# Optimization experiments

Measured on AMD Instinct MI355X. Metric: run time of the kernel, lower is better.

The kernel has to match this reference:

```python
import jax, jax.numpy as jnp
import numpy as np

L = 4096   # num_tokens (one prefill sequence)
D = 2048   # hidden_size
HK = 16    # num_k_heads
HV = 32    # num_v_heads
DK = 128   # head_k_dim
DV = 128   # head_v_dim
RATIO = HV // HK
EPS = 1e-6


def setup_inputs() -> dict:
    key = jax.random.key(0)
    ks = jax.random.split(key, 11)
    s = 0.02
    return {
        "hidden_states": jax.random.normal(ks[0], (L, D), jnp.float32),
        "Wq": jax.random.normal(ks[1], (D, HK * DK), jnp.float32) * s,
        "Wk": jax.random.normal(ks[2], (D, HK * DK), jnp.float32) * s,
        "Wv": jax.random.normal(ks[3], (D, HV * DV), jnp.float32) * s,
        "Wz": jax.random.normal(ks[4], (D, HV * DV), jnp.float32) * s,
        "Wb": jax.random.normal(ks[5], (D, HV), jnp.float32) * s,
        "Wa": jax.random.normal(ks[6], (D, HV), jnp.float32) * s,
        "A_log": jnp.log(jax.random.uniform(ks[7], (HV,), jnp.float32, 1.0, 16.0)),
        "dt_bias": jax.random.normal(ks[8], (HV,), jnp.float32) * 0.5,
        "norm_weight": jnp.ones((DV,), jnp.float32),
        "W_out": jax.random.normal(ks[9], (HV * DV, D), jnp.float32) * s,
    }


def _l2norm(x):
    return x * jax.lax.rsqrt(jnp.sum(x * x, axis=-1, keepdims=True) + EPS)


def reference(hidden_states, Wq, Wk, Wv, Wz, Wb, Wa, A_log, dt_bias, norm_weight, W_out):
    h = hidden_states
    # --- input projections (qkvz + ba split) ---
    q = _l2norm((h @ Wq).reshape(L, HK, DK))            # [L, HK, DK]
    k = _l2norm((h @ Wk).reshape(L, HK, DK))
    v = (h @ Wv).reshape(L, HV, DV)                     # [L, HV, DV]
    z = (h @ Wz).reshape(L, HV, DV)                     # gate for RMSNorm
    beta = jax.nn.sigmoid(h @ Wb)                       # [L, HV]
    g = -jnp.exp(A_log) * jax.nn.softplus(h @ Wa + dt_bias)  # [L, HV]
    decay = jnp.exp(g)                                  # per-token per-head decay
    # repeat shared q/k heads to value heads (GQA ratio)
    q = jnp.repeat(q, RATIO, axis=1) * (DK ** -0.5)     # [L, HV, DK]
    k = jnp.repeat(k, RATIO, axis=1)

    # --- gated delta rule recurrence over tokens ---
    def step(S, xs):
        q_t, k_t, v_t, b_t, d_t = xs                    # [HV,DK],[HV,DK],[HV,DV],[HV],[HV]
        S = S * d_t[:, None, None]                      # decay state [HV, DK, DV]
        pred = jnp.einsum('hk,hkv->hv', k_t, S)         # memory readout
        delta = (v_t - pred) * b_t[:, None]             # delta-rule correction
        S = S + k_t[:, :, None] * delta[:, None, :]
        o = jnp.einsum('hk,hkv->hv', q_t, S)
        return S, o

    S0 = jnp.zeros((HV, DK, DV), jnp.float32)
    _, core = jax.lax.scan(step, S0, (q, k, v, beta, decay))  # core: [L, HV, DV]

    # --- gated RMSNorm: x * silu(z), rms-normalize over head dim ---
    x = core * jax.nn.silu(z)
    x = x * jax.lax.rsqrt(jnp.mean(x * x, axis=-1, keepdims=True) + EPS) * norm_weight

    # --- output projection ---
    return x.reshape(L, HV * DV) @ W_out                # [L, D]
```

## Files before the change

kernel.cpp:

```cpp
#include <hip/hip_runtime.h>

#define LTOK 4096
#define DHID 2048
#define HKN  16
#define HVN  32
#define DKK  128
#define NTOT 12288

typedef unsigned short u16;
typedef __attribute__((ext_vector_type(8))) short short8;
typedef __attribute__((ext_vector_type(8))) unsigned short u16x8;
typedef __attribute__((ext_vector_type(4))) unsigned short u16x4;
typedef __attribute__((ext_vector_type(4))) float f32x4;

__device__ __forceinline__ float b2f(u16 u) {
  unsigned int x = ((unsigned int)u) << 16;
  return __builtin_bit_cast(float, x);
}
__device__ __forceinline__ u16 f2bf(float f) {
  unsigned int u = __builtin_bit_cast(unsigned int, f);
  u += 0x7FFFu + ((u >> 16) & 1u);
  return (u16)(u >> 16);
}

template<int C> __device__ __forceinline__ float dppmv(float x) {
  int i = __builtin_amdgcn_update_dpp(0, __builtin_bit_cast(int, x), C, 0xF, 0xF, true);
  return __builtin_bit_cast(float, i);
}
__device__ __forceinline__ float red16(float x) {
  x += dppmv<0xB1>(x);
  x += dppmv<0x4E>(x);
  x += dppmv<0x124>(x);
  x += dppmv<0x128>(x);
  return x;
}

__device__ __forceinline__ void gld16(const void* g, void* l) {
  __builtin_amdgcn_global_load_lds((const __attribute__((address_space(1))) void*)g,
                                   (__attribute__((address_space(3))) void*)l, 16, 0, 0);
}

template<int OFF> __device__ __forceinline__ short8 dsr(unsigned a) {
  short8 r;
  asm volatile("ds_read_b128 %0, %1 offset:%2" : "=v"(r) : "v"(a), "n"(OFF));
  return r;
}
__device__ __forceinline__ short8 gldx4(const u16* p) {
  short8 r;
  asm volatile("global_load_dwordx4 %0, %1, off" : "=v"(r) : "v"(p));
  return r;
}
#define KEEPV(x) asm volatile("" :: "v"(x))

__device__ __forceinline__ int sw16(int r, int c, int rowc) { return (r * rowc + c) ^ ((r & 7) << 3); }

__device__ __forceinline__ void cstore(u16* C, size_t i, float v) { C[i] = f2bf(v); }
__device__ __forceinline__ void cstore(float* C, size_t i, float v) { C[i] = v; }

__global__ __launch_bounds__(256)
void k_cvt(const float* __restrict__ s, u16* __restrict__ d, int n) {
  const int i = (blockIdx.x * 256 + threadIdx.x) * 4;
  const float4 v = *(const float4*)(s + i);
  ushort4 o;
  o.x = f2bf(v.x); o.y = f2bf(v.y); o.z = f2bf(v.z); o.w = f2bf(v.w);
  *(ushort4*)(d + i) = o;
}

__global__ __launch_bounds__(256)
void k_trf(const float* __restrict__ W, u16* __restrict__ Bf, int Ncols, int nkt, int j16base) {
  const int wv = threadIdx.x >> 6, lane = threadIdx.x & 63;
  const int frag = blockIdx.x * 4 + wv;
  const int j16 = frag / nkt, kt = frag % nkt;
  const int r0 = kt * 32 + (lane >> 4) * 8;
  const int c = j16 * 16 + (lane & 15);
  u16x8 o;
#pragma unroll
  for (int e = 0; e < 8; ++e) o[e] = f2bf(W[(size_t)(r0 + e) * Ncols + c]);
  *(u16x8*)(Bf + ((size_t)(j16base + j16) * nkt + kt) * 512 + lane * 8) = o;
}

#define MFMA16(a, b, c) __builtin_amdgcn_mfma_f32_16x16x32_bf16(a, b, c, 0, 0, 0)

template<typename OutT, int NWM, int NWN>
__global__ __launch_bounds__(NWM * 256, 2)
void k_g256(const u16* __restrict__ A, const u16* __restrict__ Bf, OutT* __restrict__ C,
            int M, int N, int K, int NT) {
  constexpr int BN = NWN * 64;
  constexpr int BUFE = NWM * 4096;
  __shared__ u16 Lds[4 * BUFE];
  const int tid = threadIdx.x;
  const int lane = tid & 63, w = tid >> 6;
  const int fr = lane & 15, fq = lane >> 4;
  const int wm = (w >> 2) * 128, wn = (w & 3) * (NWN * 16);
  const int nkt = K >> 5;
  const size_t sK = (size_t)K;

  const int MT = gridDim.x / NT;
  const int nts = (NT < 16) ? NT : 16;
  const int per_super = MT * nts;
  const int super = blockIdx.x / per_super;
  const int within = blockIdx.x % per_super;
  const int mtg = MT >> 3;
  const int q = within >> 3;
  const int mt = (within & 7) * mtg + (q % mtg);
  const int nt = super * nts + q / mtg;

  const int kslot = ((tid & 3) ^ ((tid >> 3) & 3)) * 8;
  const u16* aS = A + (size_t)(mt * (NWM * 128) + (tid >> 2)) * sK + kslot;

  const int jw = nt * (BN / 16) + (w & 3) * NWN;
  const u16* bp[NWN];
#pragma unroll
  for (int j = 0; j < NWN; ++j) bp[j] = Bf + ((size_t)(jw + j) * nkt) * 512 + lane * 8;

  f32x4 acc[8][NWN] = {};

  auto STAGE = [&](int kt_) {
    const int sk = (kt_ < nkt) ? kt_ : nkt - 1;
    u16* base = &Lds[(kt_ & 3) * BUFE];
    gld16(aS + (size_t)sk * 32, base + tid * 8);
    gld16(aS + (size_t)(NWM * 64) * sK + (size_t)sk * 32, base + NWM * 2048 + tid * 8);
  };

#define LOADB(bset, kt_) {                                                    \
    const int sk2 = ((kt_) < nkt) ? (kt_) : (nkt - 1);                        \
    _Pragma("unroll")                                                         \
    for (int j = 0; j < NWN; ++j) bset[j] = gldx4(bp[j] + (size_t)sk2 * 512); }

  const int akey = (fr >> 1) & 3;
  const unsigned ldsBase = (unsigned)(size_t)(__attribute__((address_space(3))) void*)&Lds[0];
  const unsigned aA0 = ldsBase + 2u * (unsigned)((wm + fr) * 32 + ((fq ^ akey) << 3));

  short8 afA[8], afB[8], bs0[NWN], bs1[NWN];

#define RD(afX, kt_) {                                                        \
    const unsigned aAr = aA0 + (unsigned)(((kt_) & 3) * (BUFE * 2));          \
    afX[0] = dsr<0>(aAr);    afX[1] = dsr<1024>(aAr);                         \
    afX[2] = dsr<2048>(aAr); afX[3] = dsr<3072>(aAr);                         \
    afX[4] = dsr<4096>(aAr); afX[5] = dsr<5120>(aAr);                         \
    afX[6] = dsr<6144>(aAr); afX[7] = dsr<7168>(aAr); }

  STAGE(0); STAGE(1); STAGE(2);
  LOADB(bs0, 0)
  LOADB(bs1, 1)
  asm volatile("s_waitcnt vmcnt(0)" ::: "memory");
  __builtin_amdgcn_s_barrier();
  RD(afA, 0)
  asm volatile("s_waitcnt lgkmcnt(0)" ::: "memory");
  __builtin_amdgcn_sched_barrier(0);

#define ITER(kt_, afC, bC, afN) {                                             \
    STAGE((kt_) + 3);                                                         \
    asm volatile("s_waitcnt vmcnt(%0)" :: "n"(NWN + 4) : "memory");           \
    __builtin_amdgcn_s_barrier();                                             \
    __builtin_amdgcn_sched_barrier(0);                                        \
    RD(afN, (kt_) + 1)                                                        \
    __builtin_amdgcn_sched_barrier(0);                                        \
    __builtin_amdgcn_s_setprio(1);                                            \
    _Pragma("unroll")                                                         \
    for (int i = 0; i < 8; ++i)                                               \
      _Pragma("unroll")                                                       \
      for (int j = 0; j < NWN; ++j)                                           \
        acc[i][j] = MFMA16(afC[i], bC[j], acc[i][j]);                         \
    __builtin_amdgcn_s_setprio(0);                                            \
    LOADB(bC, (kt_) + 2)                                                      \
    asm volatile("s_waitcnt lgkmcnt(0)" ::: "memory");                        \
    __builtin_amdgcn_sched_barrier(0); }

  for (int kt = 0; kt < nkt; kt += 2) {
    ITER(kt, afA, bs0, afB)
    ITER(kt + 1, afB, bs1, afA)
  }
#undef ITER
#undef RD
#undef LOADB

  asm volatile("s_waitcnt vmcnt(0) lgkmcnt(0)" ::: "memory");
  __builtin_amdgcn_sched_barrier(0);
  KEEPV(bs0[0]); KEEPV(bs0[1]);
  if constexpr (NWN == 4) { KEEPV(bs0[2]); KEEPV(bs0[3]); }
  KEEPV(bs1[0]); KEEPV(bs1[1]);
  if constexpr (NWN == 4) { KEEPV(bs1[2]); KEEPV(bs1[3]); }
  KEEPV(afA[0]); KEEPV(afA[1]); KEEPV(afA[2]); KEEPV(afA[3]);
  KEEPV(afA[4]); KEEPV(afA[5]); KEEPV(afA[6]); KEEPV(afA[7]);
  KEEPV(afB[0]); KEEPV(afB[1]); KEEPV(afB[2]); KEEPV(afB[3]);
  KEEPV(afB[4]); KEEPV(afB[5]); KEEPV(afB[6]); KEEPV(afB[7]);

  const int r0 = mt * (NWM * 128) + wm + fq * 4;
  const int c0 = nt * BN + wn + fr;
#pragma unroll
  for (int i = 0; i < 8; ++i)
#pragma unroll
    for (int j = 0; j < NWN; ++j)
#pragma unroll
      for (int e = 0; e < 4; ++e)
        cstore(C, (size_t)(r0 + i * 16 + e) * N + c0 + j * 16, acc[i][j][e]);
}

__global__ __launch_bounds__(256)
void k_ba(const float* __restrict__ h, const float* __restrict__ Wb, const float* __restrict__ Wa,
          const float* __restrict__ A_log, const float* __restrict__ dtb,
          float* __restrict__ beta, float* __restrict__ g_out) {
  const int w = threadIdx.x >> 6, lane = threadIdx.x & 63;
  const int t = blockIdx.x * 4 + w;
  const int j = lane & 31;
  const bool isB = lane < 32;
  const float* __restrict__ hr = h + (size_t)t * DHID;
  const float* Wc = isB ? Wb : Wa;
  float acc = 0.f;
  for (int kk = 0; kk < DHID; ++kk) acc = fmaf(hr[kk], Wc[(size_t)kk * HVN + j], acc);
  if (isB) {
    beta[(size_t)t * HVN + j] = 1.f / (1.f + expf(-acc));
  } else {
    float xx = acc + dtb[j];
    float sp = (xx > 20.f) ? xx : log1pf(expf(xx));
    g_out[(size_t)t * HVN + j] = -expf(A_log[j]) * sp;
  }
}

__global__ __launch_bounds__(256)
void k_l2n(u16* __restrict__ qkvz) {
  const int w = threadIdx.x >> 6, lane = threadIdx.x & 63;
  const int r = blockIdx.x * 4 + w;
  const int isK = r >> 16;
  const int rr = r & 65535;
  const int t = rr >> 4, hd = rr & 15;
  u16* p = qkvz + (size_t)t * NTOT + isK * 2048 + hd * DKK + lane * 2;
  float a = b2f(p[0]), b = b2f(p[1]);
  float ss = a * a + b * b;
  ss = red16(ss);
  ss += __shfl_xor(ss, 16);
  ss += __shfl_xor(ss, 32);
  const float sc = rsqrtf(ss + 1e-6f) * (isK ? 1.f : 0.08838834764831845f);
  p[0] = f2bf(a * sc); p[1] = f2bf(b * sc);
}

__global__ __launch_bounds__(256)
void k_r1(const u16* __restrict__ qkvz, const float* __restrict__ beta_g,
          const float* __restrict__ g_g, u16* __restrict__ UM_g, float* __restrict__ cumL_g) {
  const int pair = blockIdx.x;
  const int hv = pair >> 6, n = pair & 63;
  const int hk = hv >> 1;
  const int t0 = n * 64;
  const int tid = threadIdx.x, lane = tid & 63, wv = tid >> 6;
  const int fr = lane & 15, fq = lane >> 4;

  __shared__ __align__(16) u16 Xb[256 * 64];
  __shared__ __align__(16) u16 Dbuf0[64 * 64 * 2];
  __shared__ __align__(16) u16 Dbuf1[64 * 64 * 2];
  __shared__ float Lc[64];
  __shared__ float Bc[64];
  u16* Kl = Dbuf0;

  const int j = tid & 63, h = tid >> 6;
  const u16* kg = qkvz + (size_t)(t0 + j) * NTOT + 2048 + hk * DKK + h * 32;
  const u16* vg = qkvz + (size_t)(t0 + j) * NTOT + 4096 + hv * DKK + h * 32;
  u16x8 kv[4], vv[4];
#pragma unroll
  for (int i = 0; i < 4; ++i) { kv[i] = *(const u16x8*)(kg + i * 8); vv[i] = *(const u16x8*)(vg + i * 8); }
  if (tid < 64) {
    Lc[tid] = g_g[(size_t)(t0 + tid) * HVN + hv];
    Bc[tid] = beta_g[(size_t)(t0 + tid) * HVN + hv];
  }
#pragma unroll
  for (int i = 0; i < 4; ++i) *(u16x8*)&Kl[sw16(j, h * 32 + i * 8, 128)] = kv[i];
  __syncthreads();
  if (tid == 0) { float a = 0.f; for (int t = 0; t < 64; ++t) { a += Lc[t]; Lc[t] = a; } }
  __syncthreads();
  if (tid < 64) cumL_g[(size_t)pair * 64 + tid] = Lc[tid];

  {
    const float bj = Bc[j];
    const float mj = bj * __expf(Lc[j]);
#pragma unroll
    for (int i = 0; i < 4; ++i)
#pragma unroll
      for (int e = 0; e < 8; ++e) {
        int c = h * 32 + i * 8 + e;
        Xb[sw16(c, j, 64)] = f2bf(bj * b2f(vv[i][e]));
        Xb[sw16(128 + c, j, 64)] = f2bf(mj * b2f(kv[i][e]));
      }
  }
  f32x4 kk[4] = {};
#pragma unroll
  for (int ks = 0; ks < 4; ++ks) {
    short8 afr = *(const short8*)&Kl[sw16(wv * 16 + fr, ks * 32 + fq * 8, 128)];
#pragma unroll
    for (int ct = 0; ct < 4; ++ct) {
      short8 bfr = *(const short8*)&Kl[sw16(ct * 16 + fr, ks * 32 + fq * 8, 128)];
      kk[ct] = MFMA16(afr, bfr, kk[ct]);
    }
  }
  __syncthreads();

  f32x4 acc[16];
#pragma unroll
  for (int ct = 0; ct < 16; ++ct) {
    u16x4 xi = *(const u16x4*)&Xb[sw16(ct * 16 + fr, wv * 16 + fq * 4, 64)];
    acc[ct][0] = b2f(xi[0]); acc[ct][1] = b2f(xi[1]); acc[ct][2] = b2f(xi[2]); acc[ct][3] = b2f(xi[3]);
  }
#pragma unroll
  for (int ct = 0; ct < 4; ++ct) {
    const int s = ct * 16 + fr;
    u16x4 pk;
#pragma unroll
    for (int e = 0; e < 4; ++e) {
      const int t = wv * 16 + fq * 4 + e;
      float v = (s < t) ? -Bc[t] * __expf(Lc[t] - Lc[s]) * kk[ct][e] : 0.f;
      pk[e] = f2bf(v);
      Dbuf0[sw16(t, s, 64)] = pk[e];
    }
    *(u16x4*)&Dbuf0[4096 + sw16(s, wv * 16 + fq * 4, 64)] = pk;
  }
  __syncthreads();

  u16* DA = Dbuf0;
  u16* DB = Dbuf1;
  for (int stg = 0; stg < 6; ++stg) {
    u16* Dr = DA;
    u16* Dc = DA + 4096;
    short8 da0 = *(const short8*)&Dr[sw16(wv * 16 + fr, 0 + fq * 8, 64)];
    short8 da1 = *(const short8*)&Dr[sw16(wv * 16 + fr, 32 + fq * 8, 64)];
#pragma unroll
    for (int ct = 0; ct < 16; ++ct) {
      short8 b0 = *(const short8*)&Xb[sw16(ct * 16 + fr, 0 + fq * 8, 64)];
      short8 b1 = *(const short8*)&Xb[sw16(ct * 16 + fr, 32 + fq * 8, 64)];
      acc[ct] = MFMA16(da0, b0, acc[ct]);
      acc[ct] = MFMA16(da1, b1, acc[ct]);
    }
    f32x4 sq[4] = {};
    if (stg < 5) {
#pragma unroll
      for (int ct = 0; ct < 4; ++ct) {
        short8 sb0 = *(const short8*)&Dc[sw16(ct * 16 + fr, 0 + fq * 8, 64)];
        short8 sb1 = *(const short8*)&Dc[sw16(ct * 16 + fr, 32 + fq * 8, 64)];
        sq[ct] = MFMA16(da0, sb0, sq[ct]);
        sq[ct] = MFMA16(da1, sb1, sq[ct]);
      }
    }
    __syncthreads();
#pragma unroll
    for (int ct = 0; ct < 16; ++ct) {
      u16x4 pk;
      pk[0] = f2bf(acc[ct][0]); pk[1] = f2bf(acc[ct][1]); pk[2] = f2bf(acc[ct][2]); pk[3] = f2bf(acc[ct][3]);
      *(u16x4*)&Xb[sw16(ct * 16 + fr, wv * 16 + fq * 4, 64)] = pk;
    }
    if (stg < 5) {
#pragma unroll
      for (int ct = 0; ct < 4; ++ct) {
        u16x4 pk;
        pk[0] = f2bf(sq[ct][0]); pk[1] = f2bf(sq[ct][1]); pk[2] = f2bf(sq[ct][2]); pk[3] = f2bf(sq[ct][3]);
        *(u16x4*)&(DB + 4096)[sw16(ct * 16 + fr, wv * 16 + fq * 4, 64)] = pk;
#pragma unroll
        for (int e = 0; e < 4; ++e) DB[sw16(wv * 16 + fq * 4 + e, ct * 16 + fr, 64)] = pk[e];
      }
    }
    __syncthreads();
    u16* tmp = DA; DA = DB; DB = tmp;
  }

#pragma unroll
  for (int ct = 0; ct < 16; ++ct) {
    const int c = ct * 16 + fr;
#pragma unroll
    for (int e = 0; e < 4; ++e) {
      const int t = wv * 16 + fq * 4 + e;
      float v = acc[ct][e];
      if (ct >= 8) v = -v;
      UM_g[((size_t)pair * 64 + t) * 256 + c] = f2bf(v);
    }
  }
}

__global__ __launch_bounds__(512)
void k_r2(u16* __restrict__ qkvz, const u16* __restrict__ UM_g,
          const float* __restrict__ cumL_g, u16* __restrict__ o1_g) {
  const int hv = blockIdx.x >> 2, cs = blockIdx.x & 3;
  const int hk = hv >> 1;
  const int tid = threadIdx.x, lane = tid & 63, w = tid >> 6;
  const int fr = lane & 15, fq = lane >> 4;
  const int j = tid & 63, h = tid >> 6;
  const int tw = w & 3, dwv = w >> 2;

  __shared__ __align__(16) u16 Ml2[2][8192];
  __shared__ __align__(16) u16 Ql2[2][8192];
  __shared__ __align__(16) u16 Kt2[2][8192];
  __shared__ __align__(16) u16 dT[2048];
  __shared__ __align__(16) u16 SbT[4096];
  __shared__ __align__(16) u16 o1b[2048];
  __shared__ float Lc2[2][64];

  f32x4 sacc[2];
#pragma unroll
  for (int d = 0; d < 2; ++d) sacc[d] = (f32x4){0.f, 0.f, 0.f, 0.f};
  for (int i = tid; i < 4096; i += 512) SbT[i] = 0;

  u16x8 pQ0, pQ1, pK0, pK1, pM0, pM1;
  u16 pUn0, pUn1, pUn2, pUn3, pUc0, pUc1, pUc2, pUc3;
  float pL, pL63;

#define PREF(nn) {                                                            \
    const int nc = ((nn) < 64) ? (nn) : 63;                                   \
    const int pr = hv * 64 + nc; const int tt0 = nc * 64;                     \
    const u16* qg = qkvz + (size_t)(tt0 + j) * NTOT + hk * DKK + h * 16;      \
    pQ0 = *(const u16x8*)qg;          pQ1 = *(const u16x8*)(qg + 8);          \
    pK0 = *(const u16x8*)(qg + 2048); pK1 = *(const u16x8*)(qg + 2056);       \
    const u16* mg = UM_g + ((size_t)pr * 64 + j) * 256;                       \
    pM0 = *(const u16x8*)(mg + 128 + h * 16);                                 \
    pM1 = *(const u16x8*)(mg + 136 + h * 16);                                 \
    const u16* ug = UM_g + ((size_t)pr * 64 + tw * 16 + fq * 4) * 256         \
                    + cs * 32 + dwv * 16 + fr;                                \
    pUn0 = ug[0]; pUn1 = ug[256]; pUn2 = ug[512]; pUn3 = ug[768];             \
    pL = cumL_g[(size_t)pr * 64 + j]; pL63 = cumL_g[(size_t)pr * 64 + 63]; }

#define STW(b) {                                                              \
    *(u16x8*)&Ql2[b][sw16(j, h * 16, 128)] = pQ0;                             \
    *(u16x8*)&Ql2[b][sw16(j, h * 16 + 8, 128)] = pQ1;                         \
    *(u16x8*)&Ml2[b][sw16(j, h * 16, 128)] = pM0;                             \
    *(u16x8*)&Ml2[b][sw16(j, h * 16 + 8, 128)] = pM1;                         \
    const float scK = __expf(pL63 - pL);                                      \
    _Pragma("unroll")                                                         \
    for (int e = 0; e < 8; ++e) {                                             \
      Kt2[b][sw16(h * 16 + e, j, 64)] = f2bf(scK * b2f(pK0[e]));              \
      Kt2[b][sw16(h * 16 + 8 + e, j, 64)] = f2bf(scK * b2f(pK1[e]));          \
    }                                                                         \
    if (h == 0) Lc2[b][j] = pL; }

  PREF(0)
  STW(0)
  __syncthreads();

  for (int n = 0; n < 64; ++n) {
    const int cur = n & 1;
    const int pair = hv * 64 + n, t0 = n * 64;
    pUc0 = pUn0; pUc1 = pUn1; pUc2 = pUn2; pUc3 = pUn3;
    const float curL63 = pL63;
    PREF(n + 1)

    short8 amf[4], aqf[4];
#pragma unroll
    for (int ks = 0; ks < 4; ++ks) {
      amf[ks] = *(const short8*)&Ml2[cur][sw16(tw * 16 + fr, ks * 32 + fq * 8, 128)];
      aqf[ks] = *(const short8*)&Ql2[cur][sw16(tw * 16 + fr, ks * 32 + fq * 8, 128)];
    }
    float el[4];
#pragma unroll
    for (int e = 0; e < 4; ++e) el[e] = __expf(Lc2[cur][tw * 16 + fq * 4 + e]);
    {
      f32x4 dc;
      dc[0] = b2f(pUc0); dc[1] = b2f(pUc1); dc[2] = b2f(pUc2); dc[3] = b2f(pUc3);
      f32x4 oc = {};
#pragma unroll
      for (int ks = 0; ks < 4; ++ks) {
        short8 bs = *(const short8*)&SbT[sw16(dwv * 16 + fr, ks * 32 + fq * 8, 128)];
        dc = MFMA16(amf[ks], bs, dc);
        oc = MFMA16(aqf[ks], bs, oc);
      }
      u16x4 pkd;
      pkd[0] = f2bf(dc[0]); pkd[1] = f2bf(dc[1]); pkd[2] = f2bf(dc[2]); pkd[3] = f2bf(dc[3]);
      *(u16x4*)&dT[sw16(dwv * 16 + fr, tw * 16 + fq * 4, 64)] = pkd;
      u16x4 pko;
#pragma unroll
      for (int e = 0; e < 4; ++e) pko[e] = f2bf(oc[e] * el[e]);
      *(u16x4*)&o1b[sw16(dwv * 16 + fr, tw * 16 + fq * 4, 64)] = pko;
    }
    __syncthreads();

    {
      const int i = tid * 4;
      u16x4 vd = *(const u16x4*)&dT[i];
      const int f = cs * 2048 + i;
      *(u16x4*)(qkvz + (size_t)(t0 + (f >> 7)) * NTOT + 4096 + hv * DKK + (f & 127)) = vd;
      u16x4 vo = *(const u16x4*)&o1b[i];
      *(u16x4*)(o1_g + (size_t)pair * 8192 + cs * 2048 + i) = vo;
    }
    STW(cur ^ 1)
    {
      const float eC = __expf(curL63);
      short8 ak0 = *(const short8*)&Kt2[cur][sw16(w * 16 + fr, fq * 8, 64)];
      short8 ak1 = *(const short8*)&Kt2[cur][sw16(w * 16 + fr, 32 + fq * 8, 64)];
#pragma unroll
      for (int d = 0; d < 2; ++d) {
        short8 bd0 = *(const short8*)&dT[sw16(d * 16 + fr, fq * 8, 64)];
        short8 bd1 = *(const short8*)&dT[sw16(d * 16 + fr, 32 + fq * 8, 64)];
        f32x4 sa = sacc[d];
#pragma unroll
        for (int e = 0; e < 4; ++e) sa[e] *= eC;
        sa = MFMA16(ak0, bd0, sa);
        sa = MFMA16(ak1, bd1, sa);
        sacc[d] = sa;
        u16x4 pk;
        pk[0] = f2bf(sa[0]); pk[1] = f2bf(sa[1]); pk[2] = f2bf(sa[2]); pk[3] = f2bf(sa[3]);
        *(u16x4*)&SbT[sw16(d * 16 + fr, w * 16 + fq * 4, 128)] = pk;
      }
    }
    __syncthreads();
  }
#undef PREF
#undef STW
}

__global__ __launch_bounds__(512)
void k_r3(const u16* __restrict__ qkvz, const u16* __restrict__ o1_g,
          const float* __restrict__ cumL_g, const float* __restrict__ nw,
          u16* __restrict__ x) {
  const int pair = blockIdx.x, hv = pair >> 6, n = pair & 63, hk = hv >> 1, t0 = n * 64;
  const int tid = threadIdx.x, lane = tid & 63, w = tid >> 6;
  const int fr = lane & 15, fq = lane >> 4;
  const int j = tid & 63, h = tid >> 6;

  __shared__ __align__(16) u16 Ql[8192];
  __shared__ __align__(16) u16 Kl[8192];
  __shared__ __align__(16) u16 Gl[4096];
  __shared__ __align__(16) u16 dTl[8192];
  __shared__ __align__(16) u16 o1l[8192];
  __shared__ __align__(16) float of[64 * 132];
  __shared__ float Lc[64];
  __shared__ float Lw[128];

  {
    const u16* qg = qkvz + (size_t)(t0 + j) * NTOT + hk * DKK + h * 16;
    u16x8 q0 = *(const u16x8*)qg, q1 = *(const u16x8*)(qg + 8);
    u16x8 k0 = *(const u16x8*)(qg + 2048), k1 = *(const u16x8*)(qg + 2056);
    *(u16x8*)&Ql[sw16(j, h * 16, 128)] = q0;
    *(u16x8*)&Ql[sw16(j, h * 16 + 8, 128)] = q1;
    *(u16x8*)&Kl[sw16(j, h * 16, 128)] = k0;
    *(u16x8*)&Kl[sw16(j, h * 16 + 8, 128)] = k1;
  }
#pragma unroll
  for (int it = 0; it < 2; ++it) {
    const int f = ((w * 2 + it) * 64 + lane) * 8;
    gld16(qkvz + (size_t)(t0 + (f >> 7)) * NTOT + 4096 + hv * DKK + (f & 127),
          (char*)dTl + (w * 2 + it) * 1024);
    gld16(o1_g + (size_t)pair * 8192 + f, (char*)o1l + (w * 2 + it) * 1024);
  }
  if (tid < 64) Lc[tid] = cumL_g[(size_t)pair * 64 + tid];
  if (tid < 128) Lw[tid] = nw[tid];
  __syncthreads();

  const int tw = w & 3, sp = (w >> 2) * 2;
  {
    f32x4 kk0 = {}, kk1 = {};
#pragma unroll
    for (int ks = 0; ks < 4; ++ks) {
      short8 aq = *(const short8*)&Ql[sw16(tw * 16 + fr, ks * 32 + fq * 8, 128)];
      short8 b0 = *(const short8*)&Kl[sw16(sp * 16 + fr, ks * 32 + fq * 8, 128)];
      short8 b1 = *(const short8*)&Kl[sw16((sp + 1) * 16 + fr, ks * 32 + fq * 8, 128)];
      kk0 = MFMA16(aq, b0, kk0);
      kk1 = MFMA16(aq, b1, kk1);
    }
#pragma unroll
    for (int e = 0; e < 4; ++e) {
      const int t = tw * 16 + fq * 4 + e;
      const float Lt = Lc[t];
      const int s0 = sp * 16 + fr, s1 = s0 + 16;
      Gl[sw16(t, s0, 64)] = f2bf((s0 <= t) ? kk0[e] * __expf(Lt - Lc[s0]) : 0.f);
      Gl[sw16(t, s1, 64)] = f2bf((s1 <= t) ? kk1[e] * __expf(Lt - Lc[s1]) : 0.f);
    }
  }
  __syncthreads();

  {
    short8 ag0 = *(const short8*)&Gl[sw16(tw * 16 + fr, fq * 8, 64)];
    short8 ag1 = *(const short8*)&Gl[sw16(tw * 16 + fr, 32 + fq * 8, 64)];
#pragma unroll
    for (int dd = 0; dd < 4; ++dd) {
      const int d = (w >> 2) * 4 + dd;
      short8 bd0 = *(const short8*)&dTl[sw16(d * 16 + fr, fq * 8, 64)];
      short8 bd1 = *(const short8*)&dTl[sw16(d * 16 + fr, 32 + fq * 8, 64)];
      f32x4 oc = {};
      oc = MFMA16(ag0, bd0, oc);
      oc = MFMA16(ag1, bd1, oc);
#pragma unroll
      for (int e = 0; e < 4; ++e) of[(tw * 16 + fq * 4 + e) * 132 + d * 16 + fr] = oc[e];
    }
  }
  __syncthreads();

  {
    const int t = tid >> 3, q8 = tid & 7;
    const u16* zp = qkvz + (size_t)(t0 + t) * NTOT + 8192 + hv * DKK + q8 * 16;
    float xv[16];
    float ss = 0.f;
#pragma unroll
    for (int i = 0; i < 2; ++i) {
      u16x8 zv = *(const u16x8*)(zp + i * 8);
#pragma unroll
      for (int e = 0; e < 8; ++e) {
        const int dv = q8 * 16 + i * 8 + e;
        float z = b2f(zv[e]);
        float o = of[t * 132 + dv] + b2f(o1l[sw16(dv, t, 64)]);
        float xx = o * (z / (1.f + __expf(-z)));
        xv[i * 8 + e] = xx;
        ss = fmaf(xx, xx, ss);
      }
    }
    ss += __shfl_xor(ss, 1);
    ss += __shfl_xor(ss, 2);
    ss += __shfl_xor(ss, 4);
    const float scl = rsqrtf(ss * (1.f / 128.f) + 1e-6f);
    u16* xo = x + (size_t)(t0 + t) * 4096 + hv * DKK + q8 * 16;
#pragma unroll
    for (int i = 0; i < 2; ++i) {
      u16x8 pk;
#pragma unroll
      for (int e = 0; e < 8; ++e) pk[e] = f2bf(xv[i * 8 + e] * scl * Lw[q8 * 16 + i * 8 + e]);
      *(u16x8*)(xo + i * 8) = pk;
    }
  }
}

extern "C" void kernel_launch(void* const* d_in, const int* in_sizes, int n_in,
                              void* d_out, int out_size, void* d_ws, size_t ws_size,
                              hipStream_t stream) {
  const float* h    = (const float*)d_in[0];
  const float* Wq   = (const float*)d_in[1];
  const float* Wk   = (const float*)d_in[2];
  const float* Wv   = (const float*)d_in[3];
  const float* Wz   = (const float*)d_in[4];
  const float* Wb   = (const float*)d_in[5];
  const float* Wa   = (const float*)d_in[6];
  const float* Alog = (const float*)d_in[7];
  const float* dtb  = (const float*)d_in[8];
  const float* nw   = (const float*)d_in[9];
  const float* Wo   = (const float*)d_in[10];
  char* ws = (char*)d_ws;
  u16* h_bf  = (u16*)(ws);
  u16* Bfq   = (u16*)(ws + 16777216ull);
  u16* UM    = (u16*)(ws);
  u16* Bfo   = (u16*)(ws + 67108864ull);
  u16* qkvz  = (u16*)(ws + 83886080ull);
  u16* o1g   = (u16*)(ws + 184549376ull);
  u16* xbuf  = (u16*)(ws + 16777216ull);
  float* beta  = (float*)(ws + 218103808ull);
  float* g     = (float*)(ws + 218103808ull + 524288ull);
  float* cumL  = (float*)(ws + 218103808ull + 1048576ull);

  k_cvt<<<8192, 256, 0, stream>>>(h, h_bf, LTOK * DHID);
  k_trf<<<2048, 256, 0, stream>>>(Wq, Bfq, 2048, 64, 0);
  k_trf<<<2048, 256, 0, stream>>>(Wk, Bfq, 2048, 64, 128);
  k_trf<<<4096, 256, 0, stream>>>(Wv, Bfq, 4096, 64, 256);
  k_trf<<<4096, 256, 0, stream>>>(Wz, Bfq, 4096, 64, 512);
  k_trf<<<4096, 256, 0, stream>>>(Wo, Bfo, 2048, 128, 0);
  k_g256<u16, 2, 4><<<768, 512, 0, stream>>>(h_bf, Bfq, qkvz, 4096, 12288, 2048, 48);
  k_ba<<<1024, 256, 0, stream>>>(h, Wb, Wa, Alog, dtb, beta, g);
  k_l2n<<<32768, 256, 0, stream>>>(qkvz);
  k_r1<<<2048, 256, 0, stream>>>(qkvz, beta, g, UM, cumL);
  k_r2<<<128, 512, 0, stream>>>(qkvz, UM, cumL, o1g);
  k_r3<<<2048, 512, 0, stream>>>(qkvz, o1g, cumL, nw, xbuf);
  k_g256<float, 1, 2><<<512, 256, 0, stream>>>(xbuf, Bfo, (float*)d_out, 4096, 2048, 4096, 16);
}
```

Before: 808.0 us.

## Load recurrence operands straight into MFMA fragments, skipping LDS staging in k_r2

The chunked recurrence kernel stops staging Q, M and K tiles through double-buffered shared memory. Each lane now loads its MFMA fragment directly from global memory into registers, with ping-pong register sets (A/B) and the chunk loop unrolled by two. The per-token decay scale is moved from K onto a second scaled copy of the correction tile (dT2), which is algebraically equivalent. This removes the LDS write/read round trip and frees most of the shared memory, at the cost of more registers and strided scalar global loads for K.

```diff
diff --git a/kernel.cpp b/kernel.cpp
--- a/kernel.cpp
+++ b/kernel.cpp
@@ -379,125 +379,123 @@
   const int hk = hv >> 1;
   const int tid = threadIdx.x, lane = tid & 63, w = tid >> 6;
   const int fr = lane & 15, fq = lane >> 4;
-  const int j = tid & 63, h = tid >> 6;
   const int tw = w & 3, dwv = w >> 2;
 
-  __shared__ __align__(16) u16 Ml2[2][8192];
-  __shared__ __align__(16) u16 Ql2[2][8192];
-  __shared__ __align__(16) u16 Kt2[2][8192];
   __shared__ __align__(16) u16 dT[2048];
+  __shared__ __align__(16) u16 dT2[2048];
+  __shared__ __align__(16) u16 o1b[2048];
   __shared__ __align__(16) u16 SbT[4096];
-  __shared__ __align__(16) u16 o1b[2048];
-  __shared__ float Lc2[2][64];
 
   f32x4 sacc[2];
 #pragma unroll
   for (int d = 0; d < 2; ++d) sacc[d] = (f32x4){0.f, 0.f, 0.f, 0.f};
   for (int i = tid; i < 4096; i += 512) SbT[i] = 0;
 
-  u16x8 pQ0, pQ1, pK0, pK1, pM0, pM1;
-  u16 pUn0, pUn1, pUn2, pUn3, pUc0, pUc1, pUc2, pUc3;
-  float pL, pL63;
-
-#define PREF(nn) {                                                            \
+  u16x8 QA[4], MA[4], QB[4], MB[4], KA0, KA1, KB0, KB1;
+  u16 UA[4], UB[4];
+  float LA4[4], LB4[4], LA63, LB63;
+
+#define PREF(nn, Q, Mv, K0, K1, U, L4, L63v) {                                \
     const int nc = ((nn) < 64) ? (nn) : 63;                                   \
     const int pr = hv * 64 + nc; const int tt0 = nc * 64;                     \
-    const u16* qg = qkvz + (size_t)(tt0 + j) * NTOT + hk * DKK + h * 16;      \
-    pQ0 = *(const u16x8*)qg;          pQ1 = *(const u16x8*)(qg + 8);          \
-    pK0 = *(const u16x8*)(qg + 2048); pK1 = *(const u16x8*)(qg + 2056);       \
-    const u16* mg = UM_g + ((size_t)pr * 64 + j) * 256;                       \
-    pM0 = *(const u16x8*)(mg + 128 + h * 16);                                 \
-    pM1 = *(const u16x8*)(mg + 136 + h * 16);                                 \
+    const u16* qg = qkvz + (size_t)(tt0 + tw * 16 + fr) * NTOT + hk * DKK + fq * 8; \
+    Q[0] = *(const u16x8*)qg;        Q[1] = *(const u16x8*)(qg + 32);         \
+    Q[2] = *(const u16x8*)(qg + 64); Q[3] = *(const u16x8*)(qg + 96);         \
+    const u16* mg = UM_g + ((size_t)pr * 64 + tw * 16 + fr) * 256 + 128 + fq * 8; \
+    Mv[0] = *(const u16x8*)mg;        Mv[1] = *(const u16x8*)(mg + 32);       \
+    Mv[2] = *(const u16x8*)(mg + 64); Mv[3] = *(const u16x8*)(mg + 96);       \
     const u16* ug = UM_g + ((size_t)pr * 64 + tw * 16 + fq * 4) * 256         \
                     + cs * 32 + dwv * 16 + fr;                                \
-    pUn0 = ug[0]; pUn1 = ug[256]; pUn2 = ug[512]; pUn3 = ug[768];             \
-    pL = cumL_g[(size_t)pr * 64 + j]; pL63 = cumL_g[(size_t)pr * 64 + 63]; }
-
-#define STW(b) {                                                              \
-    *(u16x8*)&Ql2[b][sw16(j, h * 16, 128)] = pQ0;                             \
-    *(u16x8*)&Ql2[b][sw16(j, h * 16 + 8, 128)] = pQ1;                         \
-    *(u16x8*)&Ml2[b][sw16(j, h * 16, 128)] = pM0;                             \
-    *(u16x8*)&Ml2[b][sw16(j, h * 16 + 8, 128)] = pM1;                         \
-    const float scK = __expf(pL63 - pL);                                      \
+    U[0] = ug[0]; U[1] = ug[256]; U[2] = ug[512]; U[3] = ug[768];             \
+    const u16* kg = qkvz + (size_t)(tt0 + fq * 8) * NTOT + 2048 + hk * DKK + w * 16 + fr; \
     _Pragma("unroll")                                                         \
     for (int e = 0; e < 8; ++e) {                                             \
-      Kt2[b][sw16(h * 16 + e, j, 64)] = f2bf(scK * b2f(pK0[e]));              \
-      Kt2[b][sw16(h * 16 + 8 + e, j, 64)] = f2bf(scK * b2f(pK1[e]));          \
+      K0[e] = kg[(size_t)e * NTOT];                                           \
+      K1[e] = kg[(size_t)(32 + e) * NTOT];                                    \
     }                                                                         \
-    if (h == 0) Lc2[b][j] = pL; }
-
-  PREF(0)
-  STW(0)
-  __syncthreads();
-
-  for (int n = 0; n < 64; ++n) {
-    const int cur = n & 1;
-    const int pair = hv * 64 + n, t0 = n * 64;
-    pUc0 = pUn0; pUc1 = pUn1; pUc2 = pUn2; pUc3 = pUn3;
-    const float curL63 = pL63;
-    PREF(n + 1)
-
-    short8 amf[4], aqf[4];
-#pragma unroll
-    for (int ks = 0; ks < 4; ++ks) {
-      amf[ks] = *(const short8*)&Ml2[cur][sw16(tw * 16 + fr, ks * 32 + fq * 8, 128)];
-      aqf[ks] = *(const short8*)&Ql2[cur][sw16(tw * 16 + fr, ks * 32 + fq * 8, 128)];
-    }
-    float el[4];
-#pragma unroll
-    for (int e = 0; e < 4; ++e) el[e] = __expf(Lc2[cur][tw * 16 + fq * 4 + e]);
+    _Pragma("unroll")                                                         \
+    for (int e = 0; e < 4; ++e) L4[e] = cumL_g[(size_t)pr * 64 + tw * 16 + fq * 4 + e]; \
+    L63v = cumL_g[(size_t)pr * 64 + 63]; }
+
+#define PH1(Q, Mv, U, L4, L63v) {                                             \
+    float el[4], el2[4];                                                      \
+    _Pragma("unroll")                                                         \
+    for (int e = 0; e < 4; ++e) {                                             \
+      el[e] = __expf(L4[e]);                                                  \
+      el2[e] = __expf(L63v - L4[e]);                                          \
+    }                                                                         \
+    f32x4 dc;                                                                 \
+    dc[0] = b2f(U[0]); dc[1] = b2f(U[1]); dc[2] = b2f(U[2]); dc[3] = b2f(U[3]); \
+    f32x4 oc = {};                                                            \
+    _Pragma("unroll")                                                         \
+    for (int ks = 0; ks < 4; ++ks) {                                          \
+      short8 bs = *(const short8*)&SbT[sw16(dwv * 16 + fr, ks * 32 + fq * 8, 128)]; \
+      dc = MFMA16(__builtin_bit_cast(short8, Mv[ks]), bs, dc);                \
+      oc = MFMA16(__builtin_bit_cast(short8, Q[ks]), bs, oc);                 \
+    }                                                                         \
+    u16x4 pkd, pkd2, pko;                                                     \
+    _Pragma("unroll")                                                         \
+    for (int e = 0; e < 4; ++e) {                                             \
+      pkd[e]  = f2bf(dc[e]);                                                  \
+      pkd2[e] = f2bf(dc[e] * el2[e]);                                         \
+      pko[e]  = f2bf(oc[e] * el[e]);                                          \
+    }                                                                         \
+    *(u16x4*)&dT[sw16(dwv * 16 + fr, tw * 16 + fq * 4, 64)] = pkd;            \
+    *(u16x4*)&dT2[sw16(dwv * 16 + fr, tw * 16 + fq * 4, 64)] = pkd2;          \
+    *(u16x4*)&o1b[sw16(dwv * 16 + fr, tw * 16 + fq * 4, 64)] = pko; }
+
+#define PH2(K0, K1, L63v, t0_, pair_) {                                       \
+    {                                                                         \
+      const int i = tid * 4;                                                  \
+      u16x4 vd = *(const u16x4*)&dT[i];                                       \
+      const int f = cs * 2048 + i;                                            \
+      *(u16x4*)(qkvz + (size_t)((t0_) + (f >> 7)) * NTOT + 4096 + hv * DKK + (f & 127)) = vd; \
+      u16x4 vo = *(const u16x4*)&o1b[i];                                      \
+      *(u16x4*)(o1_g + (size_t)(pair_) * 8192 + cs * 2048 + i) = vo;          \
+    }                                                                         \
+    const float eC = __expf(L63v);                                            \
+    short8 ak0 = __builtin_bit_cast(short8, K0);                              \
+    short8 ak1 = __builtin_bit_cast(short8, K1);                              \
+    _Pragma("unroll")                                                         \
+    for (int d = 0; d < 2; ++d) {                                             \
+      short8 bd0 = *(const short8*)&dT2[sw16(d * 16 + fr, fq * 8, 64)];       \
+      short8 bd1 = *(const short8*)&dT2[sw16(d * 16 + fr, 32 + fq * 8, 64)];  \
+      f32x4 sa = sacc[d];                                                     \
+      _Pragma("unroll")                                                       \
+      for (int e = 0; e < 4; ++e) sa[e] *= eC;                                \
+      sa = MFMA16(ak0, bd0, sa);                                              \
+      sa = MFMA16(ak1, bd1, sa);                                              \
+      sacc[d] = sa;                                                           \
+      u16x4 pk;                                                               \
+      pk[0] = f2bf(sa[0]); pk[1] = f2bf(sa[1]); pk[2] = f2bf(sa[2]); pk[3] = f2bf(sa[3]); \
+      *(u16x4*)&SbT[sw16(d * 16 + fr, w * 16 + fq * 4, 128)] = pk;            \
+    }                                                                         \
+  }
+
+  PREF(0, QA, MA, KA0, KA1, UA, LA4, LA63)
+  __syncthreads();
+
+  for (int n = 0; n < 64; n += 2) {
     {
-      f32x4 dc;
-      dc[0] = b2f(pUc0); dc[1] = b2f(pUc1); dc[2] = b2f(pUc2); dc[3] = b2f(pUc3);
-      f32x4 oc = {};
-#pragma unroll
-      for (int ks = 0; ks < 4; ++ks) {
-        short8 bs = *(const short8*)&SbT[sw16(dwv * 16 + fr, ks * 32 + fq * 8, 128)];
-        dc = MFMA16(amf[ks], bs, dc);
-        oc = MFMA16(aqf[ks], bs, oc);
-      }
-      u16x4 pkd;
-      pkd[0] = f2bf(dc[0]); pkd[1] = f2bf(dc[1]); pkd[2] = f2bf(dc[2]); pkd[3] = f2bf(dc[3]);
-      *(u16x4*)&dT[sw16(dwv * 16 + fr, tw * 16 + fq * 4, 64)] = pkd;
-      u16x4 pko;
-#pragma unroll
-      for (int e = 0; e < 4; ++e) pko[e] = f2bf(oc[e] * el[e]);
-      *(u16x4*)&o1b[sw16(dwv * 16 + fr, tw * 16 + fq * 4, 64)] = pko;
-    }
-    __syncthreads();
-
+      PREF(n + 1, QB, MB, KB0, KB1, UB, LB4, LB63)
+      PH1(QA, MA, UA, LA4, LA63)
+      __syncthreads();
+      const int t0 = n * 64, pair = hv * 64 + n;
+      PH2(KA0, KA1, LA63, t0, pair)
+      __syncthreads();
+    }
     {
-      const int i = tid * 4;
-      u16x4 vd = *(const u16x4*)&dT[i];
-      const int f = cs * 2048 + i;
-      *(u16x4*)(qkvz + (size_t)(t0 + (f >> 7)) * NTOT + 4096 + hv * DKK + (f & 127)) = vd;
-      u16x4 vo = *(const u16x4*)&o1b[i];
-      *(u16x4*)(o1_g + (size_t)pair * 8192 + cs * 2048 + i) = vo;
-    }
-    STW(cur ^ 1)
-    {
-      const float eC = __expf(curL63);
-      short8 ak0 = *(const short8*)&Kt2[cur][sw16(w * 16 + fr, fq * 8, 64)];
-      short8 ak1 = *(const short8*)&Kt2[cur][sw16(w * 16 + fr, 32 + fq * 8, 64)];
-#pragma unroll
-      for (int d = 0; d < 2; ++d) {
-        short8 bd0 = *(const short8*)&dT[sw16(d * 16 + fr, fq * 8, 64)];
-        short8 bd1 = *(const short8*)&dT[sw16(d * 16 + fr, 32 + fq * 8, 64)];
-        f32x4 sa = sacc[d];
-#pragma unroll
-        for (int e = 0; e < 4; ++e) sa[e] *= eC;
-        sa = MFMA16(ak0, bd0, sa);
-        sa = MFMA16(ak1, bd1, sa);
-        sacc[d] = sa;
-        u16x4 pk;
-        pk[0] = f2bf(sa[0]); pk[1] = f2bf(sa[1]); pk[2] = f2bf(sa[2]); pk[3] = f2bf(sa[3]);
-        *(u16x4*)&SbT[sw16(d * 16 + fr, w * 16 + fq * 4, 128)] = pk;
-      }
-    }
-    __syncthreads();
+      PREF(n + 2, QA, MA, KA0, KA1, UA, LA4, LA63)
+      PH1(QB, MB, UB, LB4, LB63)
+      __syncthreads();
+      const int t0 = (n + 1) * 64, pair = hv * 64 + n + 1;
+      PH2(KB0, KB1, LB63, t0, pair)
+      __syncthreads();
+    }
   }
 #undef PREF
-#undef STW
+#undef PH1
+#undef PH2
 }
 
 __global__ __launch_bounds__(512)
```

Measured after the change: 792.8 us. About the same (-1.9%).
